# Performance work log

Measured on AMD Instinct MI355X. Metric: run time of the kernel, lower is better.

The kernel has to match this reference:

```python
import jax, jax.numpy as jnp
import numpy as np

B, N, H = 256, 768, 3072   # batch, codeword length n, num Tanner-graph edges E
CLIP = 0.999999


def _row_mask(rng, rows, cols, k):
    """Binary mask with ~k ones per row (random Tanner-graph connectivity)."""
    m = np.zeros((rows, cols), np.float32)
    idx = rng.integers(0, cols, size=(rows, k))
    m[np.arange(rows)[:, None], idx] = 1.0
    return jnp.asarray(m)


def setup_inputs() -> dict:
    key = jax.random.key(0)
    k_x, k_w, k_wo = jax.random.split(key, 3)
    rng = np.random.default_rng(0)

    # CN-update masks (frozen; CnUpdateLayer uses layer_mask directly)
    M_first = _row_mask(rng, H, N, 7)   # first_layer_mask1  [H, N]
    M_cn = _row_mask(rng, H, H, 7)      # VN2CN_mask_CNUpdate1 [H, H]
    # VN-update masks (baked into xavier-init weights, as in reset_parameters)
    M_vn = _row_mask(rng, H, H, 3)      # CN2VN_mask_VNUpdate1 [H, H]
    M_out = _row_mask(rng, N, H, 4)     # CN2VN_mask_output1   [N, H]

    # Dot_bias_matrix1 [N, H]: each edge column gets the LLR of one variable node
    bm = np.zeros((N, H), np.float32)
    bm[rng.integers(0, N, size=H), np.arange(H)] = 1.0
    bias_matrix = jnp.asarray(bm)
    channel_mask = jnp.eye(N, dtype=jnp.float32)  # Channel_LLR_mask1 [N, N]

    # 19 hidden VN layers (fc1..fc37), xavier-uniform * mask
    lim_h = float(np.sqrt(6.0 / (H + H)))
    W_vn = jax.random.uniform(k_w, (19, H, H), jnp.float32, -lim_h, lim_h) * M_vn[None]
    # output VN layer fc39, xavier-uniform * mask
    lim_o = float(np.sqrt(6.0 / (H + N)))
    W_out = jax.random.uniform(k_wo, (N, H), jnp.float32, -lim_o, lim_o) * M_out

    # 20 bias-scaling matrices, initialized to identity
    S = jnp.tile(jnp.eye(N, dtype=jnp.float32)[None], (20, 1, 1))

    x = jax.random.normal(k_x, (B, N), jnp.float32)  # channel LLRs
    return {"x": x, "W_vn": W_vn, "W_out": W_out, "S": S,
            "bias_matrix": bias_matrix, "channel_mask": channel_mask,
            "M_first": M_first, "M_cn": M_cn}


def _cn_update(x, M):
    """Per-row masked product with zero handling, done in log domain.
    y[b,i] = prod_{j: M[i,j]=1, x[b,j]!=0} x[b,j], or 0 if no masked entry is nonzero.
    """
    nz = (x != 0)
    safe = jnp.where(nz, x, 1.0)
    sumlog = jnp.log(jnp.abs(safe)) @ M.T           # [B, out] sum of log|x| over mask
    negc = (x < 0).astype(x.dtype) @ M.T            # count of negative entries
    cnt = nz.astype(x.dtype) @ M.T                  # count of nonzero masked entries
    prod = jnp.exp(sumlog) * (1.0 - 2.0 * (negc % 2.0))
    return jnp.where(cnt > 0, prod, jnp.zeros_like(prod))


def reference(x, W_vn, W_out, S, bias_matrix, channel_mask, M_first, M_cn):
    llr = x  # Channel_LLR
    h = _cn_update(jnp.tanh(0.5 * x), M_first)  # fc0

    def body(h, ws):
        W, Si = ws
        h = 2.0 * jnp.arctanh(jnp.clip(h, -CLIP, CLIP))
        h = jnp.tanh(0.5 * (h @ W.T + (llr @ Si) @ bias_matrix))  # VN update
        return _cn_update(h, M_cn), None                           # CN update

    h, _ = jax.lax.scan(body, h, (W_vn, S[:19]))  # fc1..fc38
    h = 2.0 * jnp.arctanh(jnp.clip(h, -CLIP, CLIP))
    return jax.nn.sigmoid(h @ W_out.T + (llr @ S[19]) @ channel_mask)  # fc39 + output
```

## Files before the change

### kernel.cpp

```cpp
#include <hip/hip_runtime.h>

typedef unsigned short u16c;

#define Hdim 3072
#define Ndim 768
#define Bdim 256
#define NLAYER 19
#define CLIPV 0.999999f

#define O_VN_CNT    0
#define O_FIRST_CNT 58368
#define O_CN_CNT    61440
#define O_S_CNT     64512
#define O_OUT_CNT   79872
#define O_BIAS_CNT  80640
#define O_CM_CNT    83712
#define CNT_TOTAL   84480
#define O_VN_COL    84480
#define O_VN_VAL    201216
#define O_S_COL     434688
#define O_S_VAL     496128
#define O_BIAS_ROW  557568
#define O_BIAS_VAL  569856
#define O_CM_ROW    582144
#define O_CM_VAL    585216
#define O_OUT_COL   588288
#define O_OUT_VAL   594432
#define O_CB_COL    600576
#define O_CB_VAL    658944
#define O_OB_COL    717312
#define O_OB_VAL    718080
#define ZERO_END    718848
#define O_FIRST_COL 718848
#define O_CN_COL    731136
#define WS_END      743424

#define C1 44826624u
#define C2 47185920u
#define C3 47775744u
#define C4 48365568u
#define C5 51314688u
#define C6 51904512u
#define C7 52051968u

__device__ __forceinline__ int f32_nz(float f) {
    unsigned b; __builtin_memcpy(&b, &f, 4);
    return (b & 0x7fffffffu) != 0u;
}

__device__ __forceinline__ float fast_tanh(float y) {
    float t = __expf(2.f * y);
    return 1.f - __fdividef(2.f, t + 1.f);
}

__device__ __forceinline__ float atanh2(float h) {
    h = fminf(fmaxf(h, -CLIPV), CLIPV);
    return __logf(__fdividef(1.f + h, 1.f - h));
}

__global__ __launch_bounds__(256) void fill_sentinel(int* __restrict__ p, int n) {
    int t = blockIdx.x * 256 + threadIdx.x;
    if (t < n) p[t] = 0x0C000C00;
}

template<int COLS, int CAP, typename CT>
__device__ __forceinline__ void row_scan(const float* __restrict__ src, unsigned lc,
        int* __restrict__ cnt, CT* __restrict__ colarr, float* __restrict__ valarr) {
    unsigned e = lc * 4u;
    float4 pk = *(const float4*)(src + e);
    float u[4] = {pk.x, pk.y, pk.z, pk.w};
    unsigned row = e / (unsigned)COLS;
    unsigned jb  = e - row * (unsigned)COLS;
    #pragma unroll
    for (int k = 0; k < 4; k++) {
        if (f32_nz(u[k])) {
            int slot = atomicAdd(&cnt[row], 1);
            if (slot < CAP) {
                colarr[row * CAP + slot] = (CT)(jb + k);
                if (valarr) valarr[row * CAP + slot] = u[k];
            }
        }
    }
}

template<int ROWS, int COLS, int CAP>
__device__ __forceinline__ void col_scan(const float* __restrict__ src, unsigned lc,
        int* __restrict__ cnt, int* __restrict__ rowarr, float* __restrict__ valarr) {
    unsigned e = lc * 4u;
    float4 pk = *(const float4*)(src + e);
    float u[4] = {pk.x, pk.y, pk.z, pk.w};
    constexpr unsigned MC = (unsigned)ROWS * (unsigned)COLS;
    unsigned m   = e / MC;
    unsigned rem = e - m * MC;
    unsigned r   = rem / (unsigned)COLS;
    unsigned cb  = rem - r * (unsigned)COLS;
    #pragma unroll
    for (int k = 0; k < 4; k++) {
        if (f32_nz(u[k])) {
            unsigned key = m * (unsigned)COLS + cb + k;
            int slot = atomicAdd(&cnt[key], 1);
            if (slot < CAP) {
                rowarr[key * CAP + slot] = (int)r;
                valarr[key * CAP + slot] = u[k];
            }
        }
    }
}

__global__ __launch_bounds__(256) void build_all(
        const float* __restrict__ Wvn, const float* __restrict__ Mc,
        const float* __restrict__ Mf,  const float* __restrict__ Wout,
        const float* __restrict__ S,   const float* __restrict__ bm,
        const float* __restrict__ cm,  int* __restrict__ ws) {
    unsigned c = blockIdx.x * 256u + threadIdx.x;
    if (c < C1) {
        row_scan<Hdim, 4, u16c>(Wvn, c, ws + O_VN_CNT,
            (u16c*)(ws + O_VN_COL), (float*)(ws + O_VN_VAL));
    } else if (c < C2) {
        row_scan<Hdim, 8, u16c>(Mc, c - C1, ws + O_CN_CNT,
            (u16c*)(ws + O_CN_COL), (float*)nullptr);
    } else if (c < C3) {
        row_scan<Ndim, 8, u16c>(Mf, c - C2, ws + O_FIRST_CNT,
            (u16c*)(ws + O_FIRST_COL), (float*)nullptr);
    } else if (c < C4) {
        row_scan<Hdim, 8, int>(Wout, c - C3, ws + O_OUT_CNT,
            ws + O_OUT_COL, (float*)(ws + O_OUT_VAL));
    } else if (c < C5) {
        col_scan<Ndim, Ndim, 4>(S, c - C4, ws + O_S_CNT,
            ws + O_S_COL, (float*)(ws + O_S_VAL));
    } else if (c < C6) {
        col_scan<Ndim, Hdim, 4>(bm, c - C5, ws + O_BIAS_CNT,
            ws + O_BIAS_ROW, (float*)(ws + O_BIAS_VAL));
    } else {
        col_scan<Ndim, Ndim, 4>(cm, c - C6, ws + O_CM_CNT,
            ws + O_CM_ROW, (float*)(ws + O_CM_VAL));
    }
}

__global__ __launch_bounds__(256) void compose_all(int* __restrict__ ws) {
    int id = blockIdx.x * 256 + threadIdx.x;
    const int*   s_cnt = ws + O_S_CNT;
    const int*   s_col = ws + O_S_COL;
    const float* s_val = (const float*)(ws + O_S_VAL);
    if (id < NLAYER * Hdim) {
        int l = id / Hdim, i = id - l * Hdim;
        const int*   bias_cnt = ws + O_BIAS_CNT;
        const int*   bias_row = ws + O_BIAS_ROW;
        const float* bias_val = (const float*)(ws + O_BIAS_VAL);
        int slot = 0;
        int bc = bias_cnt[i]; bc = bc < 4 ? bc : 4;
        for (int k1 = 0; k1 < bc; k1++) {
            int   r  = bias_row[i * 4 + k1];
            float bv = bias_val[i * 4 + k1];
            int base = l * Ndim + r;
            int sc = s_cnt[base]; sc = sc < 4 ? sc : 4;
            for (int k2 = 0; k2 < sc; k2++) {
                if (slot == 0) {
                    ws[O_CB_COL + id] = s_col[base * 4 + k2];
                    ((float*)(ws + O_CB_VAL))[id] = bv * s_val[base * 4 + k2];
                }
                slot++;
            }
        }
    } else if (id < NLAYER * Hdim + Ndim) {
        int m = id - NLAYER * Hdim;
        const int*   cm_cnt = ws + O_CM_CNT;
        const int*   cm_row = ws + O_CM_ROW;
        const float* cm_val = (const float*)(ws + O_CM_VAL);
        int slot = 0;
        int cc = cm_cnt[m]; cc = cc < 4 ? cc : 4;
        for (int k1 = 0; k1 < cc; k1++) {
            int   r = cm_row[m * 4 + k1];
            float v = cm_val[m * 4 + k1];
            int base = NLAYER * Ndim + r;
            int sc = s_cnt[base]; sc = sc < 4 ? sc : 4;
            for (int k2 = 0; k2 < sc; k2++) {
                if (slot == 0) {
                    ws[O_OB_COL + m] = s_col[base * 4 + k2];
                    ((float*)(ws + O_OB_VAL))[m] = v * s_val[base * 4 + k2];
                }
                slot++;
            }
        }
    }
}

__global__ __launch_bounds__(1024) void bp_main(
        const float* __restrict__ x, const int* __restrict__ ws,
        float* __restrict__ out) {
    const int b = blockIdx.x;
    const int t = threadIdx.x;

    const ushort4* vn_col4 = (const ushort4*)(ws + O_VN_COL);
    const float4*  vn_val4 = (const float4*)(ws + O_VN_VAL);
    const int*     cb_col  = ws + O_CB_COL;
    const float*   cb_val  = (const float*)(ws + O_CB_VAL);
    const int4*    fcol4   = (const int4*)(ws + O_FIRST_COL);
    const int4*    ccol4   = (const int4*)(ws + O_CN_COL);
    const int4*    ocol    = (const int4*)(ws + O_OUT_COL);
    const float4*  oval    = (const float4*)(ws + O_OUT_VAL);
    const int*     ob_col  = ws + O_OB_COL;
    const float*   ob_val  = (const float*)(ws + O_OB_VAL);

    __shared__ float A[Hdim];
    __shared__ float Bv[Hdim + 1];
    __shared__ float xrow[Ndim];

    if (t < Ndim) {
        float xv = x[b * Ndim + t];
        xrow[t] = xv;
        Bv[t] = fast_tanh(0.5f * xv);
    }
    if (t == 0) Bv[Hdim] = 0.f;
    __syncthreads();

    #pragma unroll
    for (int e = 0; e < 3; e++) {
        int i = t + e * 1024;
        int4 cc = fcol4[i];
        float p = 1.f; int nz = 0; float v;
        v = Bv[cc.x & 0xffff];          if (v != 0.f) { p *= v; nz++; }
        v = Bv[(unsigned)cc.x >> 16];   if (v != 0.f) { p *= v; nz++; }
        v = Bv[cc.y & 0xffff];          if (v != 0.f) { p *= v; nz++; }
        v = Bv[(unsigned)cc.y >> 16];   if (v != 0.f) { p *= v; nz++; }
        v = Bv[cc.z & 0xffff];          if (v != 0.f) { p *= v; nz++; }
        v = Bv[(unsigned)cc.z >> 16];   if (v != 0.f) { p *= v; nz++; }
        v = Bv[cc.w & 0xffff];          if (v != 0.f) { p *= v; nz++; }
        v = Bv[(unsigned)cc.w >> 16];   if (v != 0.f) { p *= v; nz++; }
        A[i] = nz ? atanh2(p) : 0.f;
    }
    __syncthreads();

    for (int l = 0; l < NLAYER; l++) {
        #pragma unroll
        for (int e = 0; e < 3; e++) {
            int i = t + e * 1024;
            int rb = l * Hdim + i;
            ushort4 vc = vn_col4[rb];
            float4  vv = vn_val4[rb];
            int   bc = cb_col[rb];
            float bv = cb_val[rb];
            float acc = vv.x * A[vc.x] + vv.y * A[vc.y]
                      + vv.z * A[vc.z] + vv.w * A[vc.w]
                      + bv * xrow[bc];
            Bv[i] = fast_tanh(0.5f * acc);
        }
        __syncthreads();
        #pragma unroll
        for (int e = 0; e < 3; e++) {
            int i = t + e * 1024;
            int4 cc = ccol4[i];
            float p = 1.f; int nz = 0; float v;
            v = Bv[cc.x & 0xffff];          if (v != 0.f) { p *= v; nz++; }
            v = Bv[(unsigned)cc.x >> 16];   if (v != 0.f) { p *= v; nz++; }
            v = Bv[cc.y & 0xffff];          if (v != 0.f) { p *= v; nz++; }
            v = Bv[(unsigned)cc.y >> 16];   if (v != 0.f) { p *= v; nz++; }
            v = Bv[cc.z & 0xffff];          if (v != 0.f) { p *= v; nz++; }
            v = Bv[(unsigned)cc.z >> 16];   if (v != 0.f) { p *= v; nz++; }
            v = Bv[cc.w & 0xffff];          if (v != 0.f) { p *= v; nz++; }
            v = Bv[(unsigned)cc.w >> 16];   if (v != 0.f) { p *= v; nz++; }
            A[i] = nz ? atanh2(p) : 0.f;
        }
        __syncthreads();
    }

    if (t < Ndim) {
        int m = t;
        int4   c0 = ocol[m * 2], c1 = ocol[m * 2 + 1];
        float4 v0 = oval[m * 2], v1 = oval[m * 2 + 1];
        float acc = v0.x * A[c0.x] + v0.y * A[c0.y] + v0.z * A[c0.z] + v0.w * A[c0.w]
                  + v1.x * A[c1.x] + v1.y * A[c1.y] + v1.z * A[c1.z] + v1.w * A[c1.w]
                  + ob_val[m] * xrow[ob_col[m]];
        out[b * Ndim + m] = __fdividef(1.f, 1.f + __expf(-acc));
    }
}

extern "C" void kernel_launch(void* const* d_in, const int* in_sizes, int n_in,
                              void* d_out, int out_size, void* d_ws, size_t ws_size,
                              hipStream_t stream) {
    const float* x    = (const float*)d_in[0];
    const float* Wvn  = (const float*)d_in[1];
    const float* Wout = (const float*)d_in[2];
    const float* S    = (const float*)d_in[3];
    const float* bm   = (const float*)d_in[4];
    const float* cm   = (const float*)d_in[5];
    const float* Mf   = (const float*)d_in[6];
    const float* Mc   = (const float*)d_in[7];
    int* ws = (int*)d_ws;

    hipMemsetAsync(ws, 0, (size_t)ZERO_END * 4, stream);
    {
        int n = WS_END - O_FIRST_COL;
        fill_sentinel<<<(n + 255) / 256, 256, 0, stream>>>(ws + O_FIRST_COL, n);
    }
    build_all<<<C7 / 256, 256, 0, stream>>>(Wvn, Mc, Mf, Wout, S, bm, cm, ws);
    compose_all<<<(NLAYER * Hdim + Ndim + 255) / 256, 256, 0, stream>>>(ws);
    bp_main<<<Bdim, 1024, 0, stream>>>(x, ws, (float*)d_out);
}
```

Baseline: 1.024 ms.

## Prefetch next-layer sparse weights into registers and use nontemporal loads in build

In the main decoder kernel, each layer's VN sparse column/value data is loaded into registers one layer ahead, during the current layer's compute, to hide global load latency behind the barrier. The CN and first-layer column indices are hoisted into registers once. The build kernel now handles two chunks per thread with half the grid and uses nontemporal loads for the dense weight scan. This raises register pressure in a 1024-thread block, which could cause spills.

```diff
diff --git a/kernel.cpp b/kernel.cpp
--- a/kernel.cpp
+++ b/kernel.cpp
@@ -1,6 +1,7 @@
 #include <hip/hip_runtime.h>
 
 typedef unsigned short u16c;
+typedef float nf4 __attribute__((ext_vector_type(4)));
 
 #define Hdim 3072
 #define Ndim 768
@@ -67,7 +68,7 @@
 __device__ __forceinline__ void row_scan(const float* __restrict__ src, unsigned lc,
         int* __restrict__ cnt, CT* __restrict__ colarr, float* __restrict__ valarr) {
     unsigned e = lc * 4u;
-    float4 pk = *(const float4*)(src + e);
+    nf4 pk = __builtin_nontemporal_load((const nf4*)(src + e));
     float u[4] = {pk.x, pk.y, pk.z, pk.w};
     unsigned row = e / (unsigned)COLS;
     unsigned jb  = e - row * (unsigned)COLS;
@@ -87,7 +88,7 @@
 __device__ __forceinline__ void col_scan(const float* __restrict__ src, unsigned lc,
         int* __restrict__ cnt, int* __restrict__ rowarr, float* __restrict__ valarr) {
     unsigned e = lc * 4u;
-    float4 pk = *(const float4*)(src + e);
+    nf4 pk = __builtin_nontemporal_load((const nf4*)(src + e));
     float u[4] = {pk.x, pk.y, pk.z, pk.w};
     constexpr unsigned MC = (unsigned)ROWS * (unsigned)COLS;
     unsigned m   = e / MC;
@@ -112,28 +113,31 @@
         const float* __restrict__ Mf,  const float* __restrict__ Wout,
         const float* __restrict__ S,   const float* __restrict__ bm,
         const float* __restrict__ cm,  int* __restrict__ ws) {
-    unsigned c = blockIdx.x * 256u + threadIdx.x;
-    if (c < C1) {
-        row_scan<Hdim, 4, u16c>(Wvn, c, ws + O_VN_CNT,
-            (u16c*)(ws + O_VN_COL), (float*)(ws + O_VN_VAL));
-    } else if (c < C2) {
-        row_scan<Hdim, 8, u16c>(Mc, c - C1, ws + O_CN_CNT,
-            (u16c*)(ws + O_CN_COL), (float*)nullptr);
-    } else if (c < C3) {
-        row_scan<Ndim, 8, u16c>(Mf, c - C2, ws + O_FIRST_CNT,
-            (u16c*)(ws + O_FIRST_COL), (float*)nullptr);
-    } else if (c < C4) {
-        row_scan<Hdim, 8, int>(Wout, c - C3, ws + O_OUT_CNT,
-            ws + O_OUT_COL, (float*)(ws + O_OUT_VAL));
-    } else if (c < C5) {
-        col_scan<Ndim, Ndim, 4>(S, c - C4, ws + O_S_CNT,
-            ws + O_S_COL, (float*)(ws + O_S_VAL));
-    } else if (c < C6) {
-        col_scan<Ndim, Hdim, 4>(bm, c - C5, ws + O_BIAS_CNT,
-            ws + O_BIAS_ROW, (float*)(ws + O_BIAS_VAL));
-    } else {
-        col_scan<Ndim, Ndim, 4>(cm, c - C6, ws + O_CM_CNT,
-            ws + O_CM_ROW, (float*)(ws + O_CM_VAL));
+    unsigned c = blockIdx.x * 512u + threadIdx.x;
+    #pragma unroll
+    for (int h = 0; h < 2; h++, c += 256u) {
+        if (c < C1) {
+            row_scan<Hdim, 4, u16c>(Wvn, c, ws + O_VN_CNT,
+                (u16c*)(ws + O_VN_COL), (float*)(ws + O_VN_VAL));
+        } else if (c < C2) {
+            row_scan<Hdim, 8, u16c>(Mc, c - C1, ws + O_CN_CNT,
+                (u16c*)(ws + O_CN_COL), (float*)nullptr);
+        } else if (c < C3) {
+            row_scan<Ndim, 8, u16c>(Mf, c - C2, ws + O_FIRST_CNT,
+                (u16c*)(ws + O_FIRST_COL), (float*)nullptr);
+        } else if (c < C4) {
+            row_scan<Hdim, 8, int>(Wout, c - C3, ws + O_OUT_CNT,
+                ws + O_OUT_COL, (float*)(ws + O_OUT_VAL));
+        } else if (c < C5) {
+            col_scan<Ndim, Ndim, 4>(S, c - C4, ws + O_S_CNT,
+                ws + O_S_COL, (float*)(ws + O_S_VAL));
+        } else if (c < C6) {
+            col_scan<Ndim, Hdim, 4>(bm, c - C5, ws + O_BIAS_CNT,
+                ws + O_BIAS_ROW, (float*)(ws + O_BIAS_VAL));
+        } else {
+            col_scan<Ndim, Ndim, 4>(cm, c - C6, ws + O_CM_CNT,
+                ws + O_CM_ROW, (float*)(ws + O_CM_VAL));
+        }
     }
 }
 
@@ -206,6 +210,20 @@
     __shared__ float Bv[Hdim + 1];
     __shared__ float xrow[Ndim];
 
+    int4 ccr[3], fcr[3];
+    #pragma unroll
+    for (int e = 0; e < 3; e++) {
+        ccr[e] = ccol4[t + e * 1024];
+        fcr[e] = fcol4[t + e * 1024];
+    }
+    ushort4 pvc[3]; float4 pvv[3]; int pbc[3]; float pbv[3];
+    #pragma unroll
+    for (int e = 0; e < 3; e++) {
+        int rb = t + e * 1024;
+        pvc[e] = vn_col4[rb]; pvv[e] = vn_val4[rb];
+        pbc[e] = cb_col[rb];  pbv[e] = cb_val[rb];
+    }
+
     if (t < Ndim) {
         float xv = x[b * Ndim + t];
         xrow[t] = xv;
@@ -217,7 +235,7 @@
     #pragma unroll
     for (int e = 0; e < 3; e++) {
         int i = t + e * 1024;
-        int4 cc = fcol4[i];
+        int4 cc = fcr[e];
         float p = 1.f; int nz = 0; float v;
         v = Bv[cc.x & 0xffff];          if (v != 0.f) { p *= v; nz++; }
         v = Bv[(unsigned)cc.x >> 16];   if (v != 0.f) { p *= v; nz++; }
@@ -235,21 +253,25 @@
         #pragma unroll
         for (int e = 0; e < 3; e++) {
             int i = t + e * 1024;
-            int rb = l * Hdim + i;
-            ushort4 vc = vn_col4[rb];
-            float4  vv = vn_val4[rb];
-            int   bc = cb_col[rb];
-            float bv = cb_val[rb];
+            ushort4 vc = pvc[e];
+            float4  vv = pvv[e];
             float acc = vv.x * A[vc.x] + vv.y * A[vc.y]
                       + vv.z * A[vc.z] + vv.w * A[vc.w]
-                      + bv * xrow[bc];
+                      + pbv[e] * xrow[pbc[e]];
             Bv[i] = fast_tanh(0.5f * acc);
+        }
+        int ln = (l < NLAYER - 1) ? l + 1 : l;
+        #pragma unroll
+        for (int e = 0; e < 3; e++) {
+            int rb = ln * Hdim + t + e * 1024;
+            pvc[e] = vn_col4[rb]; pvv[e] = vn_val4[rb];
+            pbc[e] = cb_col[rb];  pbv[e] = cb_val[rb];
         }
         __syncthreads();
         #pragma unroll
         for (int e = 0; e < 3; e++) {
             int i = t + e * 1024;
-            int4 cc = ccol4[i];
+            int4 cc = ccr[e];
             float p = 1.f; int nz = 0; float v;
             v = Bv[cc.x & 0xffff];          if (v != 0.f) { p *= v; nz++; }
             v = Bv[(unsigned)cc.x >> 16];   if (v != 0.f) { p *= v; nz++; }
@@ -288,12 +310,12 @@
     const float* Mc   = (const float*)d_in[7];
     int* ws = (int*)d_ws;
 
-    hipMemsetAsync(ws, 0, (size_t)ZERO_END * 4, stream);
+    (void)hipMemsetAsync(ws, 0, (size_t)ZERO_END * 4, stream);
     {
         int n = WS_END - O_FIRST_COL;
         fill_sentinel<<<(n + 255) / 256, 256, 0, stream>>>(ws + O_FIRST_COL, n);
     }
-    build_all<<<C7 / 256, 256, 0, stream>>>(Wvn, Mc, Mf, Wout, S, bm, cm, ws);
+    build_all<<<C7 / 512, 256, 0, stream>>>(Wvn, Mc, Mf, Wout, S, bm, cm, ws);
     compose_all<<<(NLAYER * Hdim + Ndim + 255) / 256, 256, 0, stream>>>(ws);
     bp_main<<<Bdim, 1024, 0, stream>>>(x, ws, (float*)d_out);
 }
```

Measured after the change: 1.003 ms. 1.02x faster.
